# Kernel optimization log

Measured on AMD Instinct MI355X. Metric: run time of the kernel, lower is better.

## Reference

```python
import jax, jax.numpy as jnp
import numpy as np


def setup_inputs() -> dict:
    key = jax.random.key(0)
    N, E, LENGTH, DIM = 50000, 800000, 128, 128
    k1, k2, k3 = jax.random.split(key, 3)
    x = jax.random.normal(k1, (N, LENGTH), dtype=jnp.float32)
    edge_index = jax.random.randint(k2, (2, E), 0, N, dtype=jnp.int32)
    W = jax.random.normal(k3, (LENGTH, DIM), dtype=jnp.float32) / np.sqrt(LENGTH).astype(np.float32)
    b = jnp.zeros((DIM,), dtype=jnp.float32)
    return {"x": x, "edge_index": edge_index, "W": W, "b": b, "length": LENGTH, "dim": DIM}


def reference(x, edge_index, W, b, length, dim):
    # GCNConv(length, dim) with default add_self_loops + symmetric normalization,
    # then ReLU and softmax over the feature axis (dim=1).
    N = x.shape[0]
    src, dst = edge_index[0], edge_index[1]  # messages flow src -> dst (PyG source_to_target)
    loop = jnp.arange(N, dtype=src.dtype)
    src = jnp.concatenate([src, loop])
    dst = jnp.concatenate([dst, loop])
    # degree (incl. self-loops) computed on destination nodes, as in PyG gcn_norm
    deg = jax.ops.segment_sum(jnp.ones(dst.shape, dtype=x.dtype), dst, num_segments=N)
    dinv = jnp.where(deg > 0, jax.lax.rsqrt(deg), 0.0)
    norm = dinv[src] * dinv[dst]  # [E+N]
    xw = x @ W  # [N, dim] -- transform before propagate (in >= out here)
    msgs = xw[src] * norm[:, None]  # [E+N, dim] gather + scale
    out = jax.ops.segment_sum(msgs, dst, num_segments=N) + b  # scatter-add
    out = jax.nn.relu(out)
    return jax.nn.softmax(out, axis=1)
```

## Files before the change

### kernel.cpp

```cpp
#include <hip/hip_runtime.h>
#include <hip/hip_bf16.h>


#define KDIM 128
#define CAP 48
#define DPAD 16

__device__ __forceinline__ unsigned short f2bf(float f) {
    union { float f; unsigned u; } v; v.f = f;
    unsigned r = v.u + 0x7fff + ((v.u >> 16) & 1);
    return (unsigned short)(r >> 16);
}
__device__ __forceinline__ float bflo(unsigned u) {
    union { unsigned u; float f; } v; v.u = u << 16; return v.f;
}
__device__ __forceinline__ float bfhi(unsigned u) {
    union { unsigned u; float f; } v; v.u = u & 0xffff0000u; return v.f;
}

__global__ __launch_bounds__(256) void fused_k(const float* __restrict__ x,
                                               const float* __restrict__ W,
                                               const int* __restrict__ src,
                                               const int* __restrict__ dst,
                                               int* __restrict__ degi,
                                               unsigned short* __restrict__ csr,
                                               unsigned short* __restrict__ xwh,
                                               int N, int E, int GB) {
    __shared__ float Xl[128 * 17];
    __shared__ float Wl[16 * 132];

    const int tid = threadIdx.x;

    if ((int)blockIdx.x >= GB) {
        int e = ((int)blockIdx.x - GB) * 256 + tid;
        if (e < E) {
            int d = dst[e];
            int s = src[e];
            int pos = atomicAdd(&degi[d * DPAD], 1);
            if (pos < CAP) csr[d * CAP + pos] = (unsigned short)s;
        }
        return;
    }

    const int tx = tid & 15;
    const int ty = tid >> 4;
    const int rbase = (int)blockIdx.x * 128;

    float acc[8][8];
#pragma unroll
    for (int j = 0; j < 8; ++j)
#pragma unroll
        for (int c = 0; c < 8; ++c) acc[j][c] = 0.f;

    for (int kc = 0; kc < KDIM; kc += 16) {
#pragma unroll
        for (int i = 0; i < 2; ++i) {
            int p = tid + 256 * i;
            int row = p >> 2;
            int c4 = p & 3;
            int gr = rbase + row;
            float4 v = make_float4(0.f, 0.f, 0.f, 0.f);
            if (gr < N) v = *(const float4*)(&x[(size_t)gr * KDIM + kc + c4 * 4]);
            float* dp = &Xl[row * 17 + c4 * 4];
            dp[0] = v.x; dp[1] = v.y; dp[2] = v.z; dp[3] = v.w;
        }
#pragma unroll
        for (int i = 0; i < 2; ++i) {
            int p = tid + 256 * i;
            int k = p >> 5;
            int c4 = p & 31;
            float4 v = *(const float4*)(&W[(size_t)(kc + k) * KDIM + c4 * 4]);
            *(float4*)(&Wl[k * 132 + c4 * 4]) = v;
        }
        __syncthreads();

#pragma unroll
        for (int k = 0; k < 16; ++k) {
            float xr[8];
#pragma unroll
            for (int j = 0; j < 8; ++j) xr[j] = Xl[(ty * 8 + j) * 17 + k];
            float4 w0 = *(const float4*)(&Wl[k * 132 + tx * 4]);
            float4 w1 = *(const float4*)(&Wl[k * 132 + tx * 4 + 64]);
#pragma unroll
            for (int j = 0; j < 8; ++j) {
                acc[j][0] += xr[j] * w0.x; acc[j][1] += xr[j] * w0.y;
                acc[j][2] += xr[j] * w0.z; acc[j][3] += xr[j] * w0.w;
                acc[j][4] += xr[j] * w1.x; acc[j][5] += xr[j] * w1.y;
                acc[j][6] += xr[j] * w1.z; acc[j][7] += xr[j] * w1.w;
            }
        }
        __syncthreads();
    }

#pragma unroll
    for (int j = 0; j < 8; ++j) {
        int gr = rbase + ty * 8 + j;
        if (gr < N) {
            ushort4 o0, o1;
            o0.x = f2bf(acc[j][0]); o0.y = f2bf(acc[j][1]);
            o0.z = f2bf(acc[j][2]); o0.w = f2bf(acc[j][3]);
            o1.x = f2bf(acc[j][4]); o1.y = f2bf(acc[j][5]);
            o1.z = f2bf(acc[j][6]); o1.w = f2bf(acc[j][7]);
            *(ushort4*)(&xwh[(size_t)gr * KDIM + tx * 4]) = o0;
            *(ushort4*)(&xwh[(size_t)gr * KDIM + tx * 4 + 64]) = o1;
        }
    }
}

__global__ void dinvc_k(const int* __restrict__ degi, int* __restrict__ degc,
                        float* __restrict__ dinvc, int N) {
    int i = blockIdx.x * blockDim.x + threadIdx.x;
    if (i < N) {
        int d = degi[i * DPAD];
        degc[i] = d;
        dinvc[i] = rsqrtf((float)(d + 1));
    }
}

__global__ __launch_bounds__(256) void gather_k(const unsigned short* __restrict__ xwh,
                                                const unsigned short* __restrict__ csr,
                                                const int* __restrict__ degc,
                                                const float* __restrict__ dinvc,
                                                const float* __restrict__ b,
                                                float* __restrict__ out, int N) {
    int node = (blockIdx.x * blockDim.x + threadIdx.x) >> 6;
    if (node >= N) return;
    int lane = threadIdx.x & 63;
    int h = lane >> 4;
    int c = lane & 15;

    int cnt = degc[node];
    int ccnt = min(cnt, CAP);
    float dn = dinvc[node];

    float a[8];
#pragma unroll
    for (int i = 0; i < 8; ++i) a[i] = 0.f;

    if (h == 0) {
        float sn = dn * dn;
        uint4 u = *(const uint4*)(&xwh[(size_t)node * KDIM + c * 8]);
        float4 b0 = *(const float4*)(&b[c * 8]);
        float4 b1 = *(const float4*)(&b[c * 8 + 4]);
        a[0] = bflo(u.x) * sn + b0.x; a[1] = bfhi(u.x) * sn + b0.y;
        a[2] = bflo(u.y) * sn + b0.z; a[3] = bfhi(u.y) * sn + b0.w;
        a[4] = bflo(u.z) * sn + b1.x; a[5] = bfhi(u.z) * sn + b1.y;
        a[6] = bflo(u.w) * sn + b1.z; a[7] = bfhi(u.w) * sn + b1.w;
    }

    int s_l = 0;
    float w_l = 0.f;
    if (lane < ccnt) {
        s_l = csr[(size_t)node * CAP + lane];
        w_l = dinvc[s_l];
    }

    int kmax = (ccnt + 3) >> 2;
#pragma unroll 4
    for (int k = 0; k < kmax; ++k) {
        int idx = 4 * k + h;
        int s = __shfl(s_l, idx);
        float nv = __shfl(w_l, idx) * dn;
        uint4 u = *(const uint4*)(&xwh[(size_t)s * KDIM + c * 8]);
        a[0] += bflo(u.x) * nv; a[1] += bfhi(u.x) * nv;
        a[2] += bflo(u.y) * nv; a[3] += bfhi(u.y) * nv;
        a[4] += bflo(u.z) * nv; a[5] += bfhi(u.z) * nv;
        a[6] += bflo(u.w) * nv; a[7] += bfhi(u.w) * nv;
    }

#pragma unroll
    for (int off = 16; off <= 32; off <<= 1) {
#pragma unroll
        for (int i = 0; i < 8; ++i) a[i] += __shfl_xor(a[i], off);
    }

    float mx = -1e30f;
#pragma unroll
    for (int i = 0; i < 8; ++i) {
        a[i] = fmaxf(a[i], 0.f);
        mx = fmaxf(mx, a[i]);
    }
#pragma unroll
    for (int off = 1; off < 16; off <<= 1) mx = fmaxf(mx, __shfl_xor(mx, off));
    float e[8], s = 0.f;
#pragma unroll
    for (int i = 0; i < 8; ++i) {
        e[i] = __expf(a[i] - mx);
        s += e[i];
    }
#pragma unroll
    for (int off = 1; off < 16; off <<= 1) s += __shfl_xor(s, off);
    float rs = 1.0f / s;
    if (h == 0) {
        float4 o0 = make_float4(e[0] * rs, e[1] * rs, e[2] * rs, e[3] * rs);
        float4 o1 = make_float4(e[4] * rs, e[5] * rs, e[6] * rs, e[7] * rs);
        *(float4*)(&out[(size_t)node * KDIM + c * 8]) = o0;
        *(float4*)(&out[(size_t)node * KDIM + c * 8 + 4]) = o1;
    }
}

extern "C" void kernel_launch(void* const* d_in, const int* in_sizes, int n_in,
                              void* d_out, int out_size, void* d_ws, size_t ws_size,
                              hipStream_t stream) {
    const float* x  = (const float*)d_in[0];
    const int*   ei = (const int*)d_in[1];
    const float* W  = (const float*)d_in[2];
    const float* b  = (const float*)d_in[3];

    const int N = in_sizes[0] / KDIM;
    const int E = in_sizes[1] / 2;
    const int* src = ei;
    const int* dst = ei + E;

    unsigned short* xwh   = (unsigned short*)d_ws;
    int*            degi  = (int*)(xwh + (size_t)N * KDIM);
    unsigned short* csr   = (unsigned short*)(degi + (size_t)N * DPAD);
    int*            degc  = (int*)(csr + (size_t)N * CAP);
    float*          dinvc = (float*)(degc + N);
    float*          out   = (float*)d_out;

    hipMemsetAsync(degi, 0, (size_t)N * DPAD * sizeof(int), stream);

    const int GB = (N + 127) / 128;
    const int FB = (E + 255) / 256;
    fused_k<<<GB + FB, 256, 0, stream>>>(x, W, src, dst, degi, csr, xwh, N, E, GB);

    dinvc_k<<<(N + 255) / 256, 256, 0, stream>>>(degi, degc, dinvc, N);

    gather_k<<<(N + 3) / 4, 256, 0, stream>>>(xwh, csr, degc, dinvc, b, out, N);
}
```

Before: 161.8 us.

## Split XW into two feature-half planes and partition edge atomics by destination residue

The bf16 XW matrix is stored as two column-half planes (64 features each), and the gather kernel processes each half in a separate pass with 8 lanes per neighbor and 8 neighbors in flight. The edge-build blocks now each scan a 2048-edge chunk and handle only destinations with a given residue mod 8, and the degree padding is doubled, to reduce atomic contention and false sharing. The gather passes are meant to make each half-plane more cache-resident, at the cost of reading dst eight times and running two passes over neighbors.

Result: slower. 184.8 us (+14.2%).

```diff
diff --git a/kernel.cpp b/kernel.cpp
--- a/kernel.cpp
+++ b/kernel.cpp
@@ -4,7 +4,7 @@
 
 #define KDIM 128
 #define CAP 48
-#define DPAD 16
+#define DPAD 32
 
 __device__ __forceinline__ unsigned short f2bf(float f) {
     union { float f; unsigned u; } v; v.f = f;
@@ -32,12 +32,18 @@
     const int tid = threadIdx.x;
 
     if ((int)blockIdx.x >= GB) {
-        int e = ((int)blockIdx.x - GB) * 256 + tid;
-        if (e < E) {
-            int d = dst[e];
-            int s = src[e];
-            int pos = atomicAdd(&degi[d * DPAD], 1);
-            if (pos < CAP) csr[d * CAP + pos] = (unsigned short)s;
+        int f = (int)blockIdx.x - GB;
+        int w = f >> 3;
+        int p = f & 7;
+        int base = w * 2048;
+        int lim = min(E, base + 2048);
+        for (int i = base + tid; i < lim; i += 256) {
+            int d = dst[i];
+            if ((d & 7) == p) {
+                int s = src[i];
+                int pos = atomicAdd(&degi[d * DPAD], 1);
+                if (pos < CAP) csr[d * CAP + pos] = (unsigned short)s;
+            }
         }
         return;
     }
@@ -92,6 +98,7 @@
         __syncthreads();
     }
 
+    const size_t N64 = (size_t)N * 64;
 #pragma unroll
     for (int j = 0; j < 8; ++j) {
         int gr = rbase + ty * 8 + j;
@@ -101,8 +108,8 @@
             o0.z = f2bf(acc[j][2]); o0.w = f2bf(acc[j][3]);
             o1.x = f2bf(acc[j][4]); o1.y = f2bf(acc[j][5]);
             o1.z = f2bf(acc[j][6]); o1.w = f2bf(acc[j][7]);
-            *(ushort4*)(&xwh[(size_t)gr * KDIM + tx * 4]) = o0;
-            *(ushort4*)(&xwh[(size_t)gr * KDIM + tx * 4 + 64]) = o1;
+            *(ushort4*)(&xwh[(size_t)gr * 64 + tx * 4]) = o0;
+            *(ushort4*)(&xwh[N64 + (size_t)gr * 64 + tx * 4]) = o1;
         }
     }
 }
@@ -126,27 +133,14 @@
     int node = (blockIdx.x * blockDim.x + threadIdx.x) >> 6;
     if (node >= N) return;
     int lane = threadIdx.x & 63;
-    int h = lane >> 4;
-    int c = lane & 15;
+    int slot = lane >> 3;
+    int c = lane & 7;
+
+    const size_t N64 = (size_t)N * 64;
 
     int cnt = degc[node];
     int ccnt = min(cnt, CAP);
     float dn = dinvc[node];
-
-    float a[8];
-#pragma unroll
-    for (int i = 0; i < 8; ++i) a[i] = 0.f;
-
-    if (h == 0) {
-        float sn = dn * dn;
-        uint4 u = *(const uint4*)(&xwh[(size_t)node * KDIM + c * 8]);
-        float4 b0 = *(const float4*)(&b[c * 8]);
-        float4 b1 = *(const float4*)(&b[c * 8 + 4]);
-        a[0] = bflo(u.x) * sn + b0.x; a[1] = bfhi(u.x) * sn + b0.y;
-        a[2] = bflo(u.y) * sn + b0.z; a[3] = bfhi(u.y) * sn + b0.w;
-        a[4] = bflo(u.z) * sn + b1.x; a[5] = bfhi(u.z) * sn + b1.y;
-        a[6] = bflo(u.w) * sn + b1.z; a[7] = bfhi(u.w) * sn + b1.w;
-    }
 
     int s_l = 0;
     float w_l = 0.f;
@@ -155,47 +149,90 @@
         w_l = dinvc[s_l];
     }
 
-    int kmax = (ccnt + 3) >> 2;
-#pragma unroll 4
+    const int kmax = (ccnt + 7) >> 3;
+    float a0[8], a1[8];
+#pragma unroll
+    for (int i = 0; i < 8; ++i) { a0[i] = 0.f; a1[i] = 0.f; }
+
+#pragma unroll 2
     for (int k = 0; k < kmax; ++k) {
-        int idx = 4 * k + h;
+        int idx = 8 * k + slot;
         int s = __shfl(s_l, idx);
         float nv = __shfl(w_l, idx) * dn;
-        uint4 u = *(const uint4*)(&xwh[(size_t)s * KDIM + c * 8]);
-        a[0] += bflo(u.x) * nv; a[1] += bfhi(u.x) * nv;
-        a[2] += bflo(u.y) * nv; a[3] += bfhi(u.y) * nv;
-        a[4] += bflo(u.z) * nv; a[5] += bfhi(u.z) * nv;
-        a[6] += bflo(u.w) * nv; a[7] += bfhi(u.w) * nv;
-    }
-
-#pragma unroll
-    for (int off = 16; off <= 32; off <<= 1) {
-#pragma unroll
-        for (int i = 0; i < 8; ++i) a[i] += __shfl_xor(a[i], off);
+        uint4 u = *(const uint4*)(&xwh[(size_t)s * 64 + c * 8]);
+        a0[0] += bflo(u.x) * nv; a0[1] += bfhi(u.x) * nv;
+        a0[2] += bflo(u.y) * nv; a0[3] += bfhi(u.y) * nv;
+        a0[4] += bflo(u.z) * nv; a0[5] += bfhi(u.z) * nv;
+        a0[6] += bflo(u.w) * nv; a0[7] += bfhi(u.w) * nv;
+    }
+    if (slot == 0) {
+        float sn = dn * dn;
+        uint4 u = *(const uint4*)(&xwh[(size_t)node * 64 + c * 8]);
+        float4 v0 = *(const float4*)(&b[c * 8]);
+        float4 v1 = *(const float4*)(&b[c * 8 + 4]);
+        a0[0] += bflo(u.x) * sn + v0.x; a0[1] += bfhi(u.x) * sn + v0.y;
+        a0[2] += bflo(u.y) * sn + v0.z; a0[3] += bfhi(u.y) * sn + v0.w;
+        a0[4] += bflo(u.z) * sn + v1.x; a0[5] += bfhi(u.z) * sn + v1.y;
+        a0[6] += bflo(u.w) * sn + v1.z; a0[7] += bfhi(u.w) * sn + v1.w;
+    }
+
+#pragma unroll 2
+    for (int k = 0; k < kmax; ++k) {
+        int idx = 8 * k + slot;
+        int s = __shfl(s_l, idx);
+        float nv = __shfl(w_l, idx) * dn;
+        uint4 u = *(const uint4*)(&xwh[N64 + (size_t)s * 64 + c * 8]);
+        a1[0] += bflo(u.x) * nv; a1[1] += bfhi(u.x) * nv;
+        a1[2] += bflo(u.y) * nv; a1[3] += bfhi(u.y) * nv;
+        a1[4] += bflo(u.z) * nv; a1[5] += bfhi(u.z) * nv;
+        a1[6] += bflo(u.w) * nv; a1[7] += bfhi(u.w) * nv;
+    }
+    if (slot == 0) {
+        float sn = dn * dn;
+        uint4 u = *(const uint4*)(&xwh[N64 + (size_t)node * 64 + c * 8]);
+        float4 v0 = *(const float4*)(&b[64 + c * 8]);
+        float4 v1 = *(const float4*)(&b[64 + c * 8 + 4]);
+        a1[0] += bflo(u.x) * sn + v0.x; a1[1] += bfhi(u.x) * sn + v0.y;
+        a1[2] += bflo(u.y) * sn + v0.z; a1[3] += bfhi(u.y) * sn + v0.w;
+        a1[4] += bflo(u.z) * sn + v1.x; a1[5] += bfhi(u.z) * sn + v1.y;
+        a1[6] += bflo(u.w) * sn + v1.z; a1[7] += bfhi(u.w) * sn + v1.w;
+    }
+
+#pragma unroll
+    for (int off = 8; off <= 32; off <<= 1) {
+#pragma unroll
+        for (int i = 0; i < 8; ++i) {
+            a0[i] += __shfl_xor(a0[i], off);
+            a1[i] += __shfl_xor(a1[i], off);
+        }
     }
 
     float mx = -1e30f;
 #pragma unroll
     for (int i = 0; i < 8; ++i) {
-        a[i] = fmaxf(a[i], 0.f);
-        mx = fmaxf(mx, a[i]);
-    }
-#pragma unroll
-    for (int off = 1; off < 16; off <<= 1) mx = fmaxf(mx, __shfl_xor(mx, off));
-    float e[8], s = 0.f;
+        a0[i] = fmaxf(a0[i], 0.f); mx = fmaxf(mx, a0[i]);
+        a1[i] = fmaxf(a1[i], 0.f); mx = fmaxf(mx, a1[i]);
+    }
+#pragma unroll
+    for (int off = 1; off < 8; off <<= 1) mx = fmaxf(mx, __shfl_xor(mx, off));
+    float e0[8], e1[8], s = 0.f;
 #pragma unroll
     for (int i = 0; i < 8; ++i) {
-        e[i] = __expf(a[i] - mx);
-        s += e[i];
-    }
-#pragma unroll
-    for (int off = 1; off < 16; off <<= 1) s += __shfl_xor(s, off);
+        e0[i] = __expf(a0[i] - mx); s += e0[i];
+        e1[i] = __expf(a1[i] - mx); s += e1[i];
+    }
+#pragma unroll
+    for (int off = 1; off < 8; off <<= 1) s += __shfl_xor(s, off);
     float rs = 1.0f / s;
-    if (h == 0) {
-        float4 o0 = make_float4(e[0] * rs, e[1] * rs, e[2] * rs, e[3] * rs);
-        float4 o1 = make_float4(e[4] * rs, e[5] * rs, e[6] * rs, e[7] * rs);
-        *(float4*)(&out[(size_t)node * KDIM + c * 8]) = o0;
-        *(float4*)(&out[(size_t)node * KDIM + c * 8 + 4]) = o1;
+    if (slot == 0) {
+        float4 o00 = make_float4(e0[0] * rs, e0[1] * rs, e0[2] * rs, e0[3] * rs);
+        float4 o01 = make_float4(e0[4] * rs, e0[5] * rs, e0[6] * rs, e0[7] * rs);
+        float4 o10 = make_float4(e1[0] * rs, e1[1] * rs, e1[2] * rs, e1[3] * rs);
+        float4 o11 = make_float4(e1[4] * rs, e1[5] * rs, e1[6] * rs, e1[7] * rs);
+        *(float4*)(&out[(size_t)node * KDIM + c * 8]) = o00;
+        *(float4*)(&out[(size_t)node * KDIM + c * 8 + 4]) = o01;
+        *(float4*)(&out[(size_t)node * KDIM + 64 + c * 8]) = o10;
+        *(float4*)(&out[(size_t)node * KDIM + 64 + c * 8 + 4]) = o11;
     }
 }
 
@@ -222,7 +259,7 @@
     hipMemsetAsync(degi, 0, (size_t)N * DPAD * sizeof(int), stream);
 
     const int GB = (N + 127) / 128;
-    const int FB = (E + 255) / 256;
+    const int FB = ((E + 2047) / 2048) * 8;
     fused_k<<<GB + FB, 256, 0, stream>>>(x, W, src, dst, degi, csr, xwh, N, E, GB);
 
     dinvc_k<<<(N + 255) / 256, 256, 0, stream>>>(degi, degc, dinvc, N);
```
